# Optimization experiments

Hardware: AMD Instinct MI355X
Metric: run time of the kernel (lower is better)

## Reference

```python
import jax, jax.numpy as jnp
import numpy as np
from jax import lax

VOCAB, EM, UNITS, B, T = 32000, 256, 512, 64, 16


def setup_inputs() -> dict:
    key = jax.random.key(0)
    ks = jax.random.split(key, 8)
    return {
        "inputs": jax.random.randint(ks[0], (B, T), 0, VOCAB),
        "enc_h": jax.random.normal(ks[1], (B, UNITS), jnp.float32),
        "enc_c": jax.random.normal(ks[2], (B, UNITS), jnp.float32),
        "emb_table": jax.random.normal(ks[3], (VOCAB, EM), jnp.float32) * 0.02,
        "Wx": jax.random.normal(ks[4], (EM, 4 * UNITS), jnp.float32) * 0.02,
        "Wh": jax.random.normal(ks[5], (UNITS, 4 * UNITS), jnp.float32) * 0.02,
        "b": jnp.zeros((4 * UNITS,), jnp.float32),
        "Wout": jax.random.normal(ks[6], (T * UNITS, VOCAB), jnp.float32) * 0.02,
        "bout": jnp.zeros((VOCAB,), jnp.float32),
    }


def reference(inputs, enc_h, enc_c, emb_table, Wx, Wh, b, Wout, bout):
    # Embedding lookup: [B,T,EM]. mask_zero=False -> no mask.
    em = emb_table[inputs]
    # Precompute input contribution to all gates: [T,B,4U]
    xz = (jnp.einsum('bte,eu->btu', em, Wx) + b).transpose(1, 0, 2)

    def step(carry, xz_t):
        h, c = carry
        z = xz_t + h @ Wh                     # [B,4U]
        i, f, g, o = jnp.split(z, 4, axis=-1)  # keras gate order i,f,c,o
        i = jax.nn.sigmoid(i)
        f = jax.nn.sigmoid(f)
        g = jax.nn.sigmoid(g)   # activation='sigmoid' (non-default)
        o = jax.nn.sigmoid(o)
        c = f * c + i * g
        h = o * jax.nn.sigmoid(c)  # activation='sigmoid' on cell output too
        return (h, c), h

    _, hs = lax.scan(step, (enc_h, enc_c), xz)   # hs: [T,B,U]
    flat = hs.transpose(1, 0, 2).reshape(B, T * UNITS)
    logits = flat @ Wout + bout
    return jax.nn.softmax(logits, axis=-1)
```

## Files before the change

### kernel.cpp

```cpp
#include <hip/hip_runtime.h>
#include <math.h>

#define VOCAB 32000
#define EM    256
#define UNITS 512
#define BATCH 64
#define TSTEP 16
#define G4    (4*UNITS)
#define KFLAT (TSTEP*UNITS)
#define KSPLIT 4
#define KR    (KFLAT/KSPLIT)

typedef __bf16 bf16x8 __attribute__((ext_vector_type(8)));
typedef float  f32x4  __attribute__((ext_vector_type(4)));
union FragU { __bf16 b[8]; bf16x8 v; };

__device__ __align__(16) float g_xz [TSTEP*BATCH*G4];
__device__ __align__(16) float g_ht0[UNITS*BATCH];
__device__ __align__(16) float g_ht1[UNITS*BATCH];
__device__ __align__(16) float g_c0 [BATCH*UNITS];
__device__ __align__(16) float g_c1 [BATCH*UNITS];
__device__ __align__(16) unsigned short g_Ah[BATCH*KFLAT];
__device__ __align__(16) unsigned short g_Al[BATCH*KFLAT];
__device__ __align__(16) float g_part[KSPLIT*BATCH*VOCAB];

__device__ __forceinline__ float sigmoidf_(float x) {
    return 1.0f / (1.0f + expf(-x));
}
__device__ __forceinline__ unsigned short f2bf(float f) {
    unsigned u = __float_as_uint(f);
    return (unsigned short)((u + 0x7fffu + ((u >> 16) & 1u)) >> 16);
}
__device__ __forceinline__ float bf2f(unsigned short h) {
    return __uint_as_float((unsigned)h << 16);
}

__global__ __launch_bounds__(256) void transpose_h_kernel(const float* __restrict__ src)
{
    int i = blockIdx.x * 256 + threadIdx.x;
    int b = i >> 9, u = i & 511;
    g_ht0[u*BATCH + b] = src[i];
}

__global__ __launch_bounds__(256) void xz_kernel(
    const int* __restrict__ inputs, const float* __restrict__ emb,
    const float* __restrict__ Wx, const float* __restrict__ bias)
{
    const int col = blockIdx.x * 256 + threadIdx.x;
    const int r0  = blockIdx.y * 8;
    const float* e[8];
    #pragma unroll
    for (int i = 0; i < 8; ++i) {
        int r = r0 + i, t = r >> 6, b = r & 63;
        e[i] = emb + (size_t)inputs[b*TSTEP + t]*EM;
    }
    float a[8];
    float bb = bias[col];
    #pragma unroll
    for (int i = 0; i < 8; ++i) a[i] = bb;
    #pragma unroll 2
    for (int k = 0; k < EM; ++k) {
        float w = Wx[(size_t)k*G4 + col];
        #pragma unroll
        for (int i = 0; i < 8; ++i) a[i] = fmaf(e[i][k], w, a[i]);
    }
    #pragma unroll
    for (int i = 0; i < 8; ++i)
        g_xz[(size_t)(r0+i)*G4 + col] = a[i];
}

__global__ __launch_bounds__(256) void lstm_step_kernel(
    const float* __restrict__ Wh, const float* __restrict__ enc_c, int t)
{
    const float* h_in  = (t & 1) ? g_ht1 : g_ht0;
    float*       h_out = (t & 1) ? g_ht0 : g_ht1;
    const float* c_in  = (t == 0) ? enc_c : ((t & 1) ? g_c0 : g_c1);
    float*       c_out = (t & 1) ? g_c1 : g_c0;

    __shared__ float zp[4][64][4];
    const int tid  = threadIdx.x;
    const int ci   = tid & 63, kh = tid >> 6;
    const int gate = ci >> 4, ul = ci & 15;
    const int u0   = blockIdx.x * 16;
    const int b0   = blockIdx.y * 4;
    const int col  = gate*UNITS + u0 + ul;

    float a0, a1, a2, a3;
    if (kh == 0) {
        const float* xz = g_xz + ((size_t)t*BATCH + b0)*G4 + col;
        a0 = xz[0]; a1 = xz[G4]; a2 = xz[2*G4]; a3 = xz[3*G4];
    } else {
        a0 = a1 = a2 = a3 = 0.f;
    }
    const int k0 = kh * 128;
    #pragma unroll 4
    for (int k = k0; k < k0 + 128; ++k) {
        float w = Wh[(size_t)k*G4 + col];
        const float4 hv = *reinterpret_cast<const float4*>(h_in + (size_t)k*BATCH + b0);
        a0 = fmaf(hv.x, w, a0);
        a1 = fmaf(hv.y, w, a1);
        a2 = fmaf(hv.z, w, a2);
        a3 = fmaf(hv.w, w, a3);
    }
    zp[kh][ci][0] = a0; zp[kh][ci][1] = a1;
    zp[kh][ci][2] = a2; zp[kh][ci][3] = a3;
    __syncthreads();

    if (tid < 64) {
        const int bl = tid >> 4, u2 = tid & 15;
        const int b = b0 + bl, u = u0 + u2;
        float zi = zp[0][0*16+u2][bl] + zp[1][0*16+u2][bl] + zp[2][0*16+u2][bl] + zp[3][0*16+u2][bl];
        float zf = zp[0][1*16+u2][bl] + zp[1][1*16+u2][bl] + zp[2][1*16+u2][bl] + zp[3][1*16+u2][bl];
        float zg = zp[0][2*16+u2][bl] + zp[1][2*16+u2][bl] + zp[2][2*16+u2][bl] + zp[3][2*16+u2][bl];
        float zo = zp[0][3*16+u2][bl] + zp[1][3*16+u2][bl] + zp[2][3*16+u2][bl] + zp[3][3*16+u2][bl];
        float c = sigmoidf_(zf) * c_in[(size_t)b*UNITS + u] + sigmoidf_(zi) * sigmoidf_(zg);
        float h = sigmoidf_(zo) * sigmoidf_(c);
        c_out[(size_t)b*UNITS + u] = c;
        h_out[(size_t)u*BATCH + b] = h;
        unsigned short hh = f2bf(h);
        size_t ai = (size_t)b*KFLAT + t*UNITS + u;
        g_Ah[ai] = hh;
        g_Al[ai] = f2bf(h - bf2f(hh));
    }
}

__device__ __forceinline__ void load_chunk(
    int kb, int r, int n0, const float* __restrict__ Wout,
    FragU ah[4], FragU al[4], float wB[2][8])
{
    #pragma unroll
    for (int ms = 0; ms < 4; ++ms) {
        size_t aoff = (size_t)(ms*16 + r)*KFLAT + kb;
        ah[ms].v = *reinterpret_cast<const bf16x8*>(g_Ah + aoff);
        al[ms].v = *reinterpret_cast<const bf16x8*>(g_Al + aoff);
    }
    #pragma unroll
    for (int nt = 0; nt < 2; ++nt) {
        const float* wp = Wout + (size_t)kb * VOCAB + n0 + nt*16 + r;
        #pragma unroll
        for (int j = 0; j < 8; ++j)
            wB[nt][j] = __builtin_nontemporal_load(wp + (size_t)j * VOCAB);
    }
}

__device__ __forceinline__ void compute_chunk(
    FragU ah[4], FragU al[4], float wB[2][8], f32x4 acc[4][2])
{
    #pragma unroll
    for (int nt = 0; nt < 2; ++nt) {
        FragU bh, bl;
        #pragma unroll
        for (int j = 0; j < 8; ++j) {
            float w = wB[nt][j];
            __bf16 hi = (__bf16)w;
            bh.b[j] = hi;
            bl.b[j] = (__bf16)(w - (float)hi);
        }
        #pragma unroll
        for (int ms = 0; ms < 4; ++ms)
            acc[ms][nt] = __builtin_amdgcn_mfma_f32_16x16x32_bf16(ah[ms].v, bh.v, acc[ms][nt], 0, 0, 0);
        #pragma unroll
        for (int ms = 0; ms < 4; ++ms)
            acc[ms][nt] = __builtin_amdgcn_mfma_f32_16x16x32_bf16(al[ms].v, bh.v, acc[ms][nt], 0, 0, 0);
        #pragma unroll
        for (int ms = 0; ms < 4; ++ms)
            acc[ms][nt] = __builtin_amdgcn_mfma_f32_16x16x32_bf16(ah[ms].v, bl.v, acc[ms][nt], 0, 0, 0);
    }
}

__global__ __launch_bounds__(256, 3) void logits_mfma_kernel(
    const float* __restrict__ Wout)
{
    const int tid = threadIdx.x;
    const int wv  = tid >> 6, l = tid & 63;
    const int r   = l & 15, g = l >> 4;
    const int g8  = g * 8;
    const int n0  = blockIdx.x * 128 + wv * 32;
    const int k0  = blockIdx.y * KR;

    f32x4 acc[4][2];
    #pragma unroll
    for (int ms = 0; ms < 4; ++ms)
        #pragma unroll
        for (int nt = 0; nt < 2; ++nt)
            acc[ms][nt] = (f32x4){0.f, 0.f, 0.f, 0.f};

    FragU ahA[4], alA[4]; float wA[2][8];
    FragU ahB[4], alB[4]; float wB_[2][8];

    load_chunk(k0 + g8, r, n0, Wout, ahA, alA, wA);
    for (int c = 0; c < 64; c += 2) {
        int c1 = (c+1 < 64) ? c+1 : 63;
        load_chunk(k0 + c1*32 + g8, r, n0, Wout, ahB, alB, wB_);
        compute_chunk(ahA, alA, wA, acc);
        int c2 = (c+2 < 64) ? c+2 : 63;
        load_chunk(k0 + c2*32 + g8, r, n0, Wout, ahA, alA, wA);
        compute_chunk(ahB, alB, wB_, acc);
    }

    float* pp = g_part + (size_t)blockIdx.y * BATCH * VOCAB;
    #pragma unroll
    for (int ms = 0; ms < 4; ++ms) {
        #pragma unroll
        for (int nt = 0; nt < 2; ++nt) {
            #pragma unroll
            for (int j = 0; j < 4; ++j) {
                int m = ms*16 + g*4 + j;
                pp[(size_t)m*VOCAB + n0 + nt*16 + r] = acc[ms][nt][j];
            }
        }
    }
}

__global__ __launch_bounds__(1024) void combine_softmax_kernel(
    const float* __restrict__ bout, float* __restrict__ out)
{
    const int m = blockIdx.x;
    const int tid = threadIdx.x;
    const int wid = tid >> 6, lane = tid & 63;
    __shared__ float red[16];
    float* po = out + (size_t)m * VOCAB;

    float mx = -3.0e38f;
    for (int n = tid; n < VOCAB; n += 1024) {
        float v = g_part[(size_t)0*BATCH*VOCAB + (size_t)m*VOCAB + n]
                + g_part[(size_t)1*BATCH*VOCAB + (size_t)m*VOCAB + n]
                + g_part[(size_t)2*BATCH*VOCAB + (size_t)m*VOCAB + n]
                + g_part[(size_t)3*BATCH*VOCAB + (size_t)m*VOCAB + n]
                + bout[n];
        po[n] = v;
        mx = fmaxf(mx, v);
    }
    #pragma unroll
    for (int o = 32; o; o >>= 1) mx = fmaxf(mx, __shfl_xor(mx, o));
    if (lane == 0) red[wid] = mx;
    __syncthreads();
    mx = red[0];
    #pragma unroll
    for (int i = 1; i < 16; ++i) mx = fmaxf(mx, red[i]);
    __syncthreads();

    float s = 0.f;
    for (int n = tid; n < VOCAB; n += 1024) {
        float e = expf(po[n] - mx);
        po[n] = e;
        s += e;
    }
    #pragma unroll
    for (int o = 32; o; o >>= 1) s += __shfl_xor(s, o);
    if (lane == 0) red[wid] = s;
    __syncthreads();
    s = 0.f;
    #pragma unroll
    for (int i = 0; i < 16; ++i) s += red[i];
    float inv = 1.0f / s;

    for (int n = tid; n < VOCAB; n += 1024) po[n] *= inv;
}

extern "C" void kernel_launch(void* const* d_in, const int* in_sizes, int n_in,
                              void* d_out, int out_size, void* d_ws, size_t ws_size,
                              hipStream_t stream) {
    const int*   inputs = (const int*)  d_in[0];
    const float* enc_h  = (const float*)d_in[1];
    const float* enc_c  = (const float*)d_in[2];
    const float* emb    = (const float*)d_in[3];
    const float* Wx     = (const float*)d_in[4];
    const float* Wh     = (const float*)d_in[5];
    const float* bvec   = (const float*)d_in[6];
    const float* Wout   = (const float*)d_in[7];
    const float* bout   = (const float*)d_in[8];
    float* out = (float*)d_out;
    (void)d_ws; (void)ws_size; (void)in_sizes; (void)n_in; (void)out_size;

    transpose_h_kernel<<<128, 256, 0, stream>>>(enc_h);
    xz_kernel<<<dim3(8, 128), 256, 0, stream>>>(inputs, emb, Wx, bvec);

    for (int t = 0; t < TSTEP; ++t)
        lstm_step_kernel<<<dim3(32, 16), 256, 0, stream>>>(Wh, enc_c, t);

    logits_mfma_kernel<<<dim3(250, KSPLIT), 256, 0, stream>>>(Wout);
    combine_softmax_kernel<<<64, 1024, 0, stream>>>(bout, out);
}
```

Baseline: 846.6 us.

## Drop register double-buffering in logits GEMM, double K-split and raise occupancy

Replaces the explicit two-stage register prefetch in the logits MFMA kernel with a simple per-chunk load-convert-compute loop. This frees registers so the launch bound can go from 3 to 5 blocks per CU, relying on more resident waves rather than software pipelining to hide latency. K-split is doubled to 8, which gives the grid more blocks but doubles the partial-sum buffer the combine/softmax kernel must read and write. The combine loop is generalized to sum over KSPLIT.

```diff
diff --git a/kernel.cpp b/kernel.cpp
--- a/kernel.cpp
+++ b/kernel.cpp
@@ -8,7 +8,7 @@
 #define TSTEP 16
 #define G4    (4*UNITS)
 #define KFLAT (TSTEP*UNITS)
-#define KSPLIT 4
+#define KSPLIT 8
 #define KR    (KFLAT/KSPLIT)
 
 typedef __bf16 bf16x8 __attribute__((ext_vector_type(8)));
@@ -124,51 +124,7 @@
     }
 }
 
-__device__ __forceinline__ void load_chunk(
-    int kb, int r, int n0, const float* __restrict__ Wout,
-    FragU ah[4], FragU al[4], float wB[2][8])
-{
-    #pragma unroll
-    for (int ms = 0; ms < 4; ++ms) {
-        size_t aoff = (size_t)(ms*16 + r)*KFLAT + kb;
-        ah[ms].v = *reinterpret_cast<const bf16x8*>(g_Ah + aoff);
-        al[ms].v = *reinterpret_cast<const bf16x8*>(g_Al + aoff);
-    }
-    #pragma unroll
-    for (int nt = 0; nt < 2; ++nt) {
-        const float* wp = Wout + (size_t)kb * VOCAB + n0 + nt*16 + r;
-        #pragma unroll
-        for (int j = 0; j < 8; ++j)
-            wB[nt][j] = __builtin_nontemporal_load(wp + (size_t)j * VOCAB);
-    }
-}
-
-__device__ __forceinline__ void compute_chunk(
-    FragU ah[4], FragU al[4], float wB[2][8], f32x4 acc[4][2])
-{
-    #pragma unroll
-    for (int nt = 0; nt < 2; ++nt) {
-        FragU bh, bl;
-        #pragma unroll
-        for (int j = 0; j < 8; ++j) {
-            float w = wB[nt][j];
-            __bf16 hi = (__bf16)w;
-            bh.b[j] = hi;
-            bl.b[j] = (__bf16)(w - (float)hi);
-        }
-        #pragma unroll
-        for (int ms = 0; ms < 4; ++ms)
-            acc[ms][nt] = __builtin_amdgcn_mfma_f32_16x16x32_bf16(ah[ms].v, bh.v, acc[ms][nt], 0, 0, 0);
-        #pragma unroll
-        for (int ms = 0; ms < 4; ++ms)
-            acc[ms][nt] = __builtin_amdgcn_mfma_f32_16x16x32_bf16(al[ms].v, bh.v, acc[ms][nt], 0, 0, 0);
-        #pragma unroll
-        for (int ms = 0; ms < 4; ++ms)
-            acc[ms][nt] = __builtin_amdgcn_mfma_f32_16x16x32_bf16(ah[ms].v, bl.v, acc[ms][nt], 0, 0, 0);
-    }
-}
-
-__global__ __launch_bounds__(256, 3) void logits_mfma_kernel(
+__global__ __launch_bounds__(256, 5) void logits_mfma_kernel(
     const float* __restrict__ Wout)
 {
     const int tid = threadIdx.x;
@@ -185,17 +141,33 @@
         for (int nt = 0; nt < 2; ++nt)
             acc[ms][nt] = (f32x4){0.f, 0.f, 0.f, 0.f};
 
-    FragU ahA[4], alA[4]; float wA[2][8];
-    FragU ahB[4], alB[4]; float wB_[2][8];
-
-    load_chunk(k0 + g8, r, n0, Wout, ahA, alA, wA);
-    for (int c = 0; c < 64; c += 2) {
-        int c1 = (c+1 < 64) ? c+1 : 63;
-        load_chunk(k0 + c1*32 + g8, r, n0, Wout, ahB, alB, wB_);
-        compute_chunk(ahA, alA, wA, acc);
-        int c2 = (c+2 < 64) ? c+2 : 63;
-        load_chunk(k0 + c2*32 + g8, r, n0, Wout, ahA, alA, wA);
-        compute_chunk(ahB, alB, wB_, acc);
+    for (int kk = 0; kk < KR; kk += 32) {
+        const int kb = k0 + kk + g8;
+        #pragma unroll
+        for (int nt = 0; nt < 2; ++nt) {
+            const float* wp = Wout + (size_t)kb * VOCAB + n0 + nt*16 + r;
+            float w[8];
+            #pragma unroll
+            for (int j = 0; j < 8; ++j)
+                w[j] = __builtin_nontemporal_load(wp + (size_t)j * VOCAB);
+            FragU bh, bl;
+            #pragma unroll
+            for (int j = 0; j < 8; ++j) {
+                __bf16 hi = (__bf16)w[j];
+                bh.b[j] = hi;
+                bl.b[j] = (__bf16)(w[j] - (float)hi);
+            }
+            #pragma unroll
+            for (int ms = 0; ms < 4; ++ms) {
+                size_t aoff = (size_t)(ms*16 + r)*KFLAT + kb;
+                FragU ah, al;
+                ah.v = *reinterpret_cast<const bf16x8*>(g_Ah + aoff);
+                al.v = *reinterpret_cast<const bf16x8*>(g_Al + aoff);
+                acc[ms][nt] = __builtin_amdgcn_mfma_f32_16x16x32_bf16(ah.v, bh.v, acc[ms][nt], 0, 0, 0);
+                acc[ms][nt] = __builtin_amdgcn_mfma_f32_16x16x32_bf16(al.v, bh.v, acc[ms][nt], 0, 0, 0);
+                acc[ms][nt] = __builtin_amdgcn_mfma_f32_16x16x32_bf16(ah.v, bl.v, acc[ms][nt], 0, 0, 0);
+            }
+        }
     }
 
     float* pp = g_part + (size_t)blockIdx.y * BATCH * VOCAB;
@@ -223,11 +195,10 @@
 
     float mx = -3.0e38f;
     for (int n = tid; n < VOCAB; n += 1024) {
-        float v = g_part[(size_t)0*BATCH*VOCAB + (size_t)m*VOCAB + n]
-                + g_part[(size_t)1*BATCH*VOCAB + (size_t)m*VOCAB + n]
-                + g_part[(size_t)2*BATCH*VOCAB + (size_t)m*VOCAB + n]
-                + g_part[(size_t)3*BATCH*VOCAB + (size_t)m*VOCAB + n]
-                + bout[n];
+        float v = bout[n];
+        #pragma unroll
+        for (int ks = 0; ks < KSPLIT; ++ks)
+            v += g_part[(size_t)ks*BATCH*VOCAB + (size_t)m*VOCAB + n];
         po[n] = v;
         mx = fmaxf(mx, v);
     }
```

After: 852.5 us. About the same (+0.7%).
